# Kernel optimization log

Measured on AMD Instinct MI355X. Metric: run time of the kernel, lower is better.

Reference implementation:

```python
import jax, jax.numpy as jnp
import numpy as np

EPS = 1e-6


def ln_fwd(x, gamma, beta):
    # layernorm over last dim (biased variance), per TTT ln_fwd
    mu = x.mean(-1, keepdims=True)
    var = x.var(-1, keepdims=True)
    xh = (x - mu) * jax.lax.rsqrt(var + EPS)
    return gamma * xh + beta


def ln_fused_l2_bwd(x, l2_target, gamma, beta):
    # grad of 0.5*||LN(x) - target||^2 w.r.t. x, fused (per TTT ln_fused_l2_bwd)
    D = x.shape[-1]
    mu = x.mean(-1, keepdims=True)
    var = x.var(-1, keepdims=True)
    std = jnp.sqrt(var + EPS)
    xh = (x - mu) / std
    y = gamma * xh + beta
    gxh = (y - l2_target) * gamma
    z = (D * gxh - gxh.sum(-1, keepdims=True) - xh * (gxh * xh).sum(-1, keepdims=True)) / (D * std)
    return z


def setup_inputs() -> dict:
    key = jax.random.key(0)
    ks = jax.random.split(key, 5)
    B, nh, nmb, mbs, hd = 8, 8, 256, 16, 64
    XQ = jax.random.normal(ks[0], (B, nh, nmb, mbs, hd), jnp.float32)
    XK = jax.random.normal(ks[1], (B, nh, nmb, mbs, hd), jnp.float32)
    XV = jax.random.normal(ks[2], (B, nh, nmb, mbs, hd), jnp.float32)
    # eta = small positive per-token learning rates (ttt_base_lr/head_dim scale)
    eta = jax.random.uniform(ks[3], (B, nh, nmb, mbs, mbs), jnp.float32) * (1.0 / hd)
    W1 = jax.random.normal(ks[4], (nh, hd, hd), jnp.float32) * 0.02
    b1 = jnp.zeros((nh, 1, hd), jnp.float32)
    ln_weight = jnp.ones((nh * hd,), jnp.float32)
    ln_bias = jnp.zeros((nh * hd,), jnp.float32)
    return {"XQ": XQ, "XK": XK, "XV": XV, "eta": eta, "W1": W1, "b1": b1,
            "ln_weight": ln_weight, "ln_bias": ln_bias}


def reference(XQ, XK, XV, eta, W1, b1, ln_weight, ln_bias):
    B, nh, nmb, mbs, hd = XQ.shape
    lnw = ln_weight.reshape(nh, 1, hd)
    lnb = ln_bias.reshape(nh, 1, hd)
    W1_0 = jnp.broadcast_to(W1[None], (B, nh, hd, hd))
    b1_0 = jnp.broadcast_to(b1[None], (B, nh, 1, hd))
    tril = jnp.tril(jnp.ones((mbs, mbs), XQ.dtype))

    def step(carry, inp):
        W1s, b1s = carry               # [B,nh,hd,hd], [B,nh,1,hd]
        xq, xk, xv, et = inp           # [B,nh,mbs,hd] x3, [B,nh,mbs,mbs]
        Z1 = xk @ W1s + b1s
        g = ln_fused_l2_bwd(Z1, xv - xk, lnw, lnb)          # grad_l_wrt_Z1
        Attn1 = tril * (xq @ jnp.swapaxes(xk, -1, -2))      # causal QK^T
        b1_bar = b1s - (tril * et) @ g
        Z1_bar = xq @ W1s - (et * Attn1) @ g + b1_bar
        last_eta = et[..., -1, :, None]                     # [B,nh,mbs,1]
        W1_last = W1s - jnp.swapaxes(last_eta * xk, -1, -2) @ g
        b1_last = b1s - jnp.sum(last_eta * g, axis=-2, keepdims=True)
        out = xq + ln_fwd(Z1_bar, lnw, lnb)
        return (W1_last, b1_last), out

    xs = (jnp.moveaxis(XQ, 2, 0), jnp.moveaxis(XK, 2, 0),
          jnp.moveaxis(XV, 2, 0), jnp.moveaxis(eta, 2, 0))
    _, outs = jax.lax.scan(step, (W1_0, b1_0), xs)
    # outs: [nmb,B,nh,mbs,hd] -> [B,nmb,mbs,nh,hd] -> [B,L,width]
    return jnp.transpose(outs, (1, 0, 3, 2, 4)).reshape(B, nmb * mbs, nh * hd)
```

## Files before the change

### kernel.cpp

```cpp
#include <hip/hip_runtime.h>
#include <hip/hip_bf16.h>

typedef __attribute__((ext_vector_type(8))) short short8;
typedef __attribute__((ext_vector_type(4))) short short4_t;
typedef __attribute__((ext_vector_type(4))) float f32x4;

constexpr int MBS = 16, HD = 64, NMB = 256;

#define MFMA32(a, b, c) __builtin_amdgcn_mfma_f32_16x16x32_bf16(a, b, c, 0, 0, 0)

#if __has_builtin(__builtin_amdgcn_mfma_f32_16x16x16bf16_1k)
#define MFMA16(a, b, c) __builtin_amdgcn_mfma_f32_16x16x16bf16_1k(a, b, c, 0, 0, 0)
#else
__device__ inline f32x4 mfma16_asm(short4_t a, short4_t b, f32x4 c) {
    asm volatile("v_mfma_f32_16x16x16_bf16 %0, %1, %2, %0\n\ts_nop 7\n\ts_nop 7"
                 : "+v"(c) : "v"(a), "v"(b));
    return c;
}
#define MFMA16(a, b, c) mfma16_asm(a, b, c)
#endif

#define TR_READ(dst, addr, IMM) \
    asm volatile("ds_read_b64_tr_b16 %0, %1 offset:" IMM : "=&v"(dst) : "v"(addr) : "memory")

union U2S4 { unsigned u[2]; short4_t s; };
union FI { float f; int i; };

__device__ inline unsigned pkbf(float a, float b) {
    union { __hip_bfloat162 h; unsigned u; } c;
    c.h = __float22bfloat162_rn(make_float2(a, b));
    return c.u;
}
__device__ inline short bf16s(float x) { return (short)(pkbf(x, 0.f) & 0xffffu); }
__device__ inline float dpp16(float x) {
    FI v; v.f = x; FI t;
    t.i = __builtin_amdgcn_update_dpp(0, v.i, 0xB1, 0xf, 0xf, true);  v.f += t.f;
    t.i = __builtin_amdgcn_update_dpp(0, v.i, 0x4E, 0xf, 0xf, true);  v.f += t.f;
    t.i = __builtin_amdgcn_update_dpp(0, v.i, 0x124, 0xf, 0xf, true); v.f += t.f;
    t.i = __builtin_amdgcn_update_dpp(0, v.i, 0x128, 0xf, 0xf, true); v.f += t.f;
    return v.f;
}
__device__ inline void bar() {
    __builtin_amdgcn_sched_barrier(0);
    asm volatile("s_waitcnt lgkmcnt(0)" ::: "memory");
    __builtin_amdgcn_s_barrier();
    __builtin_amdgcn_sched_barrier(0);
}

__global__ __launch_bounds__(256) void ttt_scan(
    const float* __restrict__ gXQ, const float* __restrict__ gXK,
    const float* __restrict__ gXV, const float* __restrict__ gETA,
    const float* __restrict__ gW1, const float* __restrict__ gB1,
    const float* __restrict__ gLNW, const float* __restrict__ gLNB,
    float* __restrict__ gOUT)
{
    __shared__ __align__(16) short sWt[64 * 72];
    __shared__ __align__(16) short bxk[16 * 72];
    __shared__ __align__(16) short bxq[16 * 72];
    __shared__ __align__(16) short sGt[1024];
    __shared__ __align__(16) short sXKe[1024];
    __shared__ __align__(16) short sE[16 * 20];
    __shared__ __align__(16) float sZ1[16 * 68];
    __shared__ __align__(16) float sZb[16 * 68];
    __shared__ __align__(16) float sEta[2][256];

    const int t  = threadIdx.x;
    const int s  = t >> 4;
    const int dt = t & 15;
    const int lane = t & 63;
    const int w  = t >> 6;
    const int gq = lane >> 4;
    const int lc = lane & 15;
    const int bh = blockIdx.x, b = bh >> 3, h = bh & 7;

    const float* xqg = gXQ + (size_t)bh * (NMB * MBS * HD);
    const float* xkg = gXK + (size_t)bh * (NMB * MBS * HD);
    const float* xvg = gXV + (size_t)bh * (NMB * MBS * HD);
    const float* etg = gETA + (size_t)bh * (NMB * MBS * MBS);

    f32x4 Wacc[4];
#pragma unroll
    for (int ct = 0; ct < 4; ++ct) {
#pragma unroll
        for (int r = 0; r < 4; ++r)
            Wacc[ct][r] = gW1[h * 4096 + (16 * w + 4 * gq + r) * 64 + 16 * ct + lc];
        U2S4 wp;
        wp.u[0] = pkbf(Wacc[ct][0], Wacc[ct][1]);
        wp.u[1] = pkbf(Wacc[ct][2], Wacc[ct][3]);
        *(short4_t*)&sWt[(16 * ct + lc) * 72 + 16 * w + 4 * gq] = wp.s;
    }
    float b1v = gB1[h * 64 + 16 * w + lc];

    const float4 gam = *(const float4*)&gLNW[h * 64 + dt * 4];
    const float4 bet = *(const float4*)&gLNB[h * 64 + dt * 4];
    const float ga[4] = {gam.x, gam.y, gam.z, gam.w};
    const float ba[4] = {bet.x, bet.y, bet.z, bet.w};
    float c1a[4], gba[4];
    float sc1 = 0.f;
#pragma unroll
    for (int c = 0; c < 4; ++c) {
        c1a[c] = ga[c] * ga[c];
        gba[c] = ga[c] * ba[c];
        sc1 += c1a[c];
    }
    sc1 = dpp16(sc1);

    float4 pq = *(const float4*)&xqg[t * 4];
    float4 pk = *(const float4*)&xkg[t * 4];
    float4 pv = *(const float4*)&xvg[t * 4];
    float4 pe = make_float4(0.f, 0.f, 0.f, 0.f);
    if (t < 64) pe = *(const float4*)&etg[t * 4];

    { U2S4 u_; u_.u[0]=pkbf(pk.x,pk.y); u_.u[1]=pkbf(pk.z,pk.w);
      *(short4_t*)&bxk[s * 72 + dt * 4] = u_.s; }
    { U2S4 u_; u_.u[0]=pkbf(pq.x,pq.y); u_.u[1]=pkbf(pq.z,pq.w);
      *(short4_t*)&bxq[s * 72 + dt * 4] = u_.s; }
    if (t < 64) *(float4*)&sEta[0][t * 4] = pe;
    float t2c[4];
    {
        const float pva[4] = {pv.x, pv.y, pv.z, pv.w};
        const float pka_[4] = {pk.x, pk.y, pk.z, pk.w};
#pragma unroll
        for (int c = 0; c < 4; ++c)
            t2c[c] = fmaf(-ga[c], pva[c] - pka_[c], gba[c]);
    }
    float4 pkc = pk;
    float4 pq_out = pq;
    float4 pq_prev_out;

    __syncthreads();

#pragma unroll 1
    for (int m = 0; m < NMB; ++m) {
        const int p = m & 1;

        if (m + 1 < NMB) {
            const size_t o = (size_t)(m + 1) * (MBS * HD) + t * 4;
            pq = *(const float4*)&xqg[o];
            pk = *(const float4*)&xkg[o];
            pv = *(const float4*)&xvg[o];
            if (t < 64) pe = *(const float4*)&etg[(size_t)(m + 1) * (MBS * MBS) + t * 4];
        }

        f32x4 z1a; z1a[0]=b1v; z1a[1]=b1v; z1a[2]=b1v; z1a[3]=b1v;
        f32x4 zqa = z1a;
        const short8 ak0 = *(const short8*)&bxk[lc * 72 + gq * 8];
        const short8 ak1 = *(const short8*)&bxk[lc * 72 + gq * 8 + 32];
        const short8 aq0 = *(const short8*)&bxq[lc * 72 + gq * 8];
        const short8 aq1 = *(const short8*)&bxq[lc * 72 + gq * 8 + 32];
        const short8 bw0 = *(const short8*)&sWt[(16 * w + lc) * 72 + gq * 8];
        const short8 bw1 = *(const short8*)&sWt[(16 * w + lc) * 72 + gq * 8 + 32];
        z1a = MFMA32(ak0, bw0, z1a); z1a = MFMA32(ak1, bw1, z1a);
        zqa = MFMA32(aq0, bw0, zqa); zqa = MFMA32(aq1, bw1, zqa);
#pragma unroll
        for (int r = 0; r < 4; ++r) sZ1[(4 * gq + r) * 68 + 16 * w + lc] = z1a[r];

        if (w == 3) {
            f32x4 zz; zz[0]=0.f; zz[1]=0.f; zz[2]=0.f; zz[3]=0.f;
            zz = MFMA32(aq0, ak0, zz); zz = MFMA32(aq1, ak1, zz);
#pragma unroll
            for (int r = 0; r < 4; ++r) {
                const int row = 4 * gq + r;
                const float ev = sEta[p][row * 16 + lc];
                const float x = (lc <= row) ? -ev * (1.f + zz[r]) : 0.f;
                sE[row * 20 + lc] = bf16s(x);
            }
        }

        if (m > 0) {
            f32x4 zbr = *(f32x4*)&sZb[s * 68 + dt * 4];
            float T1 = 0.f, T2 = 0.f;
#pragma unroll
            for (int c = 0; c < 4; ++c) { T1 += zbr[c]; T2 = fmaf(zbr[c], zbr[c], T2); }
            T1 = dpp16(T1); T2 = dpp16(T2);
            const float mu2   = T1 * (1.f / 64.f);
            const float rstd2 = rsqrtf(T2 * (1.f / 64.f) - mu2 * mu2 + 1e-6f);
            const float pqa[4] = {pq_prev_out.x, pq_prev_out.y, pq_prev_out.z, pq_prev_out.w};
            float o[4];
#pragma unroll
            for (int c = 0; c < 4; ++c)
                o[c] = pqa[c] + fmaf(ga[c], (zbr[c] - mu2) * rstd2, ba[c]);
            const size_t oi = ((size_t)b * 4096 + (size_t)(m - 1) * 16 + s) * 512 + h * 64 + dt * 4;
            *(float4*)&gOUT[oi] = make_float4(o[0], o[1], o[2], o[3]);
        }
        bar();

        f32x4 z = *(f32x4*)&sZ1[s * 68 + dt * 4];
        float S1=0.f,S2=0.f,S3=0.f,S4=0.f,S5=0.f,S6=0.f;
#pragma unroll
        for (int c = 0; c < 4; ++c) {
            const float zc = z[c], c1z = c1a[c] * zc, t2 = t2c[c];
            S1 += zc;  S2 = fmaf(zc, zc, S2);
            S3 += c1z; S4 = fmaf(c1z, zc, S4);
            S5 += t2;  S6 = fmaf(t2, zc, S6);
        }
        S1 = dpp16(S1); S2 = dpp16(S2); S3 = dpp16(S3);
        S4 = dpp16(S4); S5 = dpp16(S5); S6 = dpp16(S6);
        const float mu   = S1 * (1.f / 64.f);
        const float rstd = rsqrtf(S2 * (1.f / 64.f) - mu * mu + 1e-6f);
        const float r1 = rstd * (S3 - mu * sc1) + S5;
        const float r2 = rstd * rstd * (S4 - 2.f * mu * S3 + mu * mu * sc1)
                       + rstd * (S6 - mu * S5);
        const float cf = rstd * (1.f / 64.f);
        float g[4];
#pragma unroll
        for (int c = 0; c < 4; ++c) {
            const float xh = (z[c] - mu) * rstd;
            const float gx = fmaf(c1a[c], xh, t2c[c]);
            g[c] = (fmaf(64.f, gx, -r1) - xh * r2) * cf;
        }

        const float le = sEta[p][240 + s];
        const int tb = (s >> 2) * 256 + (dt >> 2) * 64 + (s & 3) * 16 + (dt & 3) * 4;
        { U2S4 gp; gp.u[0]=pkbf(g[0],g[1]); gp.u[1]=pkbf(g[2],g[3]);
          *(short4_t*)&sGt[tb] = gp.s; }
        { U2S4 kp; kp.u[0]=pkbf(-le*pkc.x,-le*pkc.y); kp.u[1]=pkbf(-le*pkc.z,-le*pkc.w);
          *(short4_t*)&sXKe[tb] = kp.s; }
        bar();

        const unsigned gbase = (unsigned)(size_t)&sGt[0] + 512u * gq + 8u * lc;
        const unsigned kbase = (unsigned)(size_t)&sXKe[0] + 512u * gq + 128u * (unsigned)w + 8u * lc;
        short4_t bg0, bg1, bg2, bg3, aK;
        TR_READ(bg0, gbase, "0");
        TR_READ(bg1, gbase, "128");
        TR_READ(bg2, gbase, "256");
        TR_READ(bg3, gbase, "384");
        TR_READ(aK,  kbase, "0");
        const short4_t aE = *(const short4_t*)&sE[lc * 20 + gq * 4];
        const f32x4 lv = *(const f32x4*)&sEta[p][240 + 4 * gq];
        U2S4 aL;
        aL.u[0] = pkbf(-lv[0], -lv[1]);
        aL.u[1] = pkbf(-lv[2], -lv[3]);
        asm volatile("s_waitcnt lgkmcnt(0)" ::: "memory");
        __builtin_amdgcn_sched_barrier(0);

        short4_t bgw = bg0;
        if (w == 1) bgw = bg1;
        else if (w == 2) bgw = bg2;
        else if (w == 3) bgw = bg3;

        f32x4 zb = MFMA16(aE, bgw, zqa);
#pragma unroll
        for (int r = 0; r < 4; ++r) sZb[(4 * gq + r) * 68 + 16 * w + lc] = zb[r];

        Wacc[0] = MFMA16(aK, bg0, Wacc[0]);
        Wacc[1] = MFMA16(aK, bg1, Wacc[1]);
        Wacc[2] = MFMA16(aK, bg2, Wacc[2]);
        Wacc[3] = MFMA16(aK, bg3, Wacc[3]);
        {
            f32x4 d0; d0[0]=0.f; d0[1]=0.f; d0[2]=0.f; d0[3]=0.f;
            d0 = MFMA16(aL.s, bgw, d0);
            b1v += d0[0];
        }
#pragma unroll
        for (int ct = 0; ct < 4; ++ct) {
            U2S4 wp;
            wp.u[0] = pkbf(Wacc[ct][0], Wacc[ct][1]);
            wp.u[1] = pkbf(Wacc[ct][2], Wacc[ct][3]);
            *(short4_t*)&sWt[(16 * ct + lc) * 72 + 16 * w + 4 * gq] = wp.s;
        }

        if (m + 1 < NMB) {
            { U2S4 u_; u_.u[0]=pkbf(pk.x,pk.y); u_.u[1]=pkbf(pk.z,pk.w);
              *(short4_t*)&bxk[s * 72 + dt * 4] = u_.s; }
            { U2S4 u_; u_.u[0]=pkbf(pq.x,pq.y); u_.u[1]=pkbf(pq.z,pq.w);
              *(short4_t*)&bxq[s * 72 + dt * 4] = u_.s; }
            if (t < 64) *(float4*)&sEta[p ^ 1][t * 4] = pe;
#pragma unroll
            for (int c = 0; c < 4; ++c) {
                const float pva[4] = {pv.x, pv.y, pv.z, pv.w};
                const float pka_[4] = {pk.x, pk.y, pk.z, pk.w};
                t2c[c] = fmaf(-ga[c], pva[c] - pka_[c], gba[c]);
            }
            pkc = pk;
        }
        pq_prev_out = pq_out;
        pq_out = pq;
        bar();
    }

    {
        f32x4 zbr = *(f32x4*)&sZb[s * 68 + dt * 4];
        float T1 = 0.f, T2 = 0.f;
#pragma unroll
        for (int c = 0; c < 4; ++c) { T1 += zbr[c]; T2 = fmaf(zbr[c], zbr[c], T2); }
        T1 = dpp16(T1); T2 = dpp16(T2);
        const float mu2   = T1 * (1.f / 64.f);
        const float rstd2 = rsqrtf(T2 * (1.f / 64.f) - mu2 * mu2 + 1e-6f);
        const float pqa[4] = {pq_prev_out.x, pq_prev_out.y, pq_prev_out.z, pq_prev_out.w};
        float o[4];
#pragma unroll
        for (int c = 0; c < 4; ++c)
            o[c] = pqa[c] + fmaf(ga[c], (zbr[c] - mu2) * rstd2, ba[c]);
        const size_t oi = ((size_t)b * 4096 + (size_t)(NMB - 1) * 16 + s) * 512 + h * 64 + dt * 4;
        *(float4*)&gOUT[oi] = make_float4(o[0], o[1], o[2], o[3]);
    }
}

extern "C" void kernel_launch(void* const* d_in, const int* in_sizes, int n_in,
                              void* d_out, int out_size, void* d_ws, size_t ws_size,
                              hipStream_t stream) {
    const float* XQ  = (const float*)d_in[0];
    const float* XK  = (const float*)d_in[1];
    const float* XV  = (const float*)d_in[2];
    const float* ETA = (const float*)d_in[3];
    const float* W1  = (const float*)d_in[4];
    const float* B1  = (const float*)d_in[5];
    const float* LNW = (const float*)d_in[6];
    const float* LNB = (const float*)d_in[7];
    float* OUT = (float*)d_out;

    const int n_chains = in_sizes[0] / (NMB * MBS * HD);
    ttt_scan<<<n_chains, 256, 0, stream>>>(XQ, XK, XV, ETA, W1, B1, LNW, LNB, OUT);
}
```

Before: 374.7 us.

## Split scan block into producer and query warp groups with 512 threads

Doubles the block to 512 threads. The first 256 threads handle the key path: the Z1 matmul, the fused LN-L2 gradient and the W1 update. The other 256 handle the query path: the XQ@W and QK^T matmuls, the eta mask, the Z1_bar MFMA and the output layernorm and store. This spreads per-chunk work that one group of warps used to do serially across more waves, so the two paths can run concurrently between barriers. In exchange it costs extra barrier participants, duplicated b1 tracking, and more register pressure under the new launch bound.

```diff
diff --git a/kernel.cpp b/kernel.cpp
--- a/kernel.cpp
+++ b/kernel.cpp
@@ -47,7 +47,7 @@
     __builtin_amdgcn_sched_barrier(0);
 }
 
-__global__ __launch_bounds__(256) void ttt_scan(
+__global__ __launch_bounds__(512) void ttt_scan(
     const float* __restrict__ gXQ, const float* __restrict__ gXK,
     const float* __restrict__ gXV, const float* __restrict__ gETA,
     const float* __restrict__ gW1, const float* __restrict__ gB1,
@@ -65,10 +65,12 @@
     __shared__ __align__(16) float sEta[2][256];
 
     const int t  = threadIdx.x;
-    const int s  = t >> 4;
-    const int dt = t & 15;
-    const int lane = t & 63;
-    const int w  = t >> 6;
+    const bool prod = (t < 256);
+    const int t4 = t & 255;
+    const int s  = t4 >> 4;
+    const int dt = t4 & 15;
+    const int lane = t4 & 63;
+    const int w  = t4 >> 6;
     const int gq = lane >> 4;
     const int lc = lane & 15;
     const int bh = blockIdx.x, b = bh >> 3, h = bh & 7;
@@ -79,15 +81,17 @@
     const float* etg = gETA + (size_t)bh * (NMB * MBS * MBS);
 
     f32x4 Wacc[4];
-#pragma unroll
-    for (int ct = 0; ct < 4; ++ct) {
-#pragma unroll
-        for (int r = 0; r < 4; ++r)
-            Wacc[ct][r] = gW1[h * 4096 + (16 * w + 4 * gq + r) * 64 + 16 * ct + lc];
-        U2S4 wp;
-        wp.u[0] = pkbf(Wacc[ct][0], Wacc[ct][1]);
-        wp.u[1] = pkbf(Wacc[ct][2], Wacc[ct][3]);
-        *(short4_t*)&sWt[(16 * ct + lc) * 72 + 16 * w + 4 * gq] = wp.s;
+    if (prod) {
+#pragma unroll
+        for (int ct = 0; ct < 4; ++ct) {
+#pragma unroll
+            for (int r = 0; r < 4; ++r)
+                Wacc[ct][r] = gW1[h * 4096 + (16 * w + 4 * gq + r) * 64 + 16 * ct + lc];
+            U2S4 wp;
+            wp.u[0] = pkbf(Wacc[ct][0], Wacc[ct][1]);
+            wp.u[1] = pkbf(Wacc[ct][2], Wacc[ct][3]);
+            *(short4_t*)&sWt[(16 * ct + lc) * 72 + 16 * w + 4 * gq] = wp.s;
+        }
     }
     float b1v = gB1[h * 64 + 16 * w + lc];
 
@@ -105,181 +109,197 @@
     }
     sc1 = dpp16(sc1);
 
-    float4 pq = *(const float4*)&xqg[t * 4];
-    float4 pk = *(const float4*)&xkg[t * 4];
-    float4 pv = *(const float4*)&xvg[t * 4];
-    float4 pe = make_float4(0.f, 0.f, 0.f, 0.f);
-    if (t < 64) pe = *(const float4*)&etg[t * 4];
-
-    { U2S4 u_; u_.u[0]=pkbf(pk.x,pk.y); u_.u[1]=pkbf(pk.z,pk.w);
-      *(short4_t*)&bxk[s * 72 + dt * 4] = u_.s; }
-    { U2S4 u_; u_.u[0]=pkbf(pq.x,pq.y); u_.u[1]=pkbf(pq.z,pq.w);
-      *(short4_t*)&bxq[s * 72 + dt * 4] = u_.s; }
-    if (t < 64) *(float4*)&sEta[0][t * 4] = pe;
-    float t2c[4];
-    {
-        const float pva[4] = {pv.x, pv.y, pv.z, pv.w};
-        const float pka_[4] = {pk.x, pk.y, pk.z, pk.w};
-#pragma unroll
-        for (int c = 0; c < 4; ++c)
-            t2c[c] = fmaf(-ga[c], pva[c] - pka_[c], gba[c]);
-    }
-    float4 pkc = pk;
-    float4 pq_out = pq;
-    float4 pq_prev_out;
-
+    float4 pk_c, pv_c, pk_n, pv_n;
+    float4 pq_c, pq_n, pq_prev, pkb_n, pe_n;
+    if (prod) {
+        pk_c = *(const float4*)&xkg[t4 * 4];
+        pv_c = *(const float4*)&xvg[t4 * 4];
+    } else {
+        pq_c = *(const float4*)&xqg[t4 * 4];
+        float4 k0 = *(const float4*)&xkg[t4 * 4];
+        { U2S4 u_; u_.u[0]=pkbf(k0.x,k0.y); u_.u[1]=pkbf(k0.z,k0.w);
+          *(short4_t*)&bxk[s * 72 + dt * 4] = u_.s; }
+        { U2S4 u_; u_.u[0]=pkbf(pq_c.x,pq_c.y); u_.u[1]=pkbf(pq_c.z,pq_c.w);
+          *(short4_t*)&bxq[s * 72 + dt * 4] = u_.s; }
+        if (t4 < 64) {
+            float4 e0 = *(const float4*)&etg[t4 * 4];
+            *(float4*)&sEta[0][t4 * 4] = e0;
+        }
+    }
     __syncthreads();
 
 #pragma unroll 1
     for (int m = 0; m < NMB; ++m) {
         const int p = m & 1;
+        f32x4 zqa, zz;
 
         if (m + 1 < NMB) {
-            const size_t o = (size_t)(m + 1) * (MBS * HD) + t * 4;
-            pq = *(const float4*)&xqg[o];
-            pk = *(const float4*)&xkg[o];
-            pv = *(const float4*)&xvg[o];
-            if (t < 64) pe = *(const float4*)&etg[(size_t)(m + 1) * (MBS * MBS) + t * 4];
-        }
-
-        f32x4 z1a; z1a[0]=b1v; z1a[1]=b1v; z1a[2]=b1v; z1a[3]=b1v;
-        f32x4 zqa = z1a;
-        const short8 ak0 = *(const short8*)&bxk[lc * 72 + gq * 8];
-        const short8 ak1 = *(const short8*)&bxk[lc * 72 + gq * 8 + 32];
-        const short8 aq0 = *(const short8*)&bxq[lc * 72 + gq * 8];
-        const short8 aq1 = *(const short8*)&bxq[lc * 72 + gq * 8 + 32];
-        const short8 bw0 = *(const short8*)&sWt[(16 * w + lc) * 72 + gq * 8];
-        const short8 bw1 = *(const short8*)&sWt[(16 * w + lc) * 72 + gq * 8 + 32];
-        z1a = MFMA32(ak0, bw0, z1a); z1a = MFMA32(ak1, bw1, z1a);
-        zqa = MFMA32(aq0, bw0, zqa); zqa = MFMA32(aq1, bw1, zqa);
-#pragma unroll
-        for (int r = 0; r < 4; ++r) sZ1[(4 * gq + r) * 68 + 16 * w + lc] = z1a[r];
-
-        if (w == 3) {
-            f32x4 zz; zz[0]=0.f; zz[1]=0.f; zz[2]=0.f; zz[3]=0.f;
-            zz = MFMA32(aq0, ak0, zz); zz = MFMA32(aq1, ak1, zz);
-#pragma unroll
-            for (int r = 0; r < 4; ++r) {
-                const int row = 4 * gq + r;
-                const float ev = sEta[p][row * 16 + lc];
-                const float x = (lc <= row) ? -ev * (1.f + zz[r]) : 0.f;
-                sE[row * 20 + lc] = bf16s(x);
-            }
-        }
-
-        if (m > 0) {
-            f32x4 zbr = *(f32x4*)&sZb[s * 68 + dt * 4];
-            float T1 = 0.f, T2 = 0.f;
-#pragma unroll
-            for (int c = 0; c < 4; ++c) { T1 += zbr[c]; T2 = fmaf(zbr[c], zbr[c], T2); }
-            T1 = dpp16(T1); T2 = dpp16(T2);
-            const float mu2   = T1 * (1.f / 64.f);
-            const float rstd2 = rsqrtf(T2 * (1.f / 64.f) - mu2 * mu2 + 1e-6f);
-            const float pqa[4] = {pq_prev_out.x, pq_prev_out.y, pq_prev_out.z, pq_prev_out.w};
-            float o[4];
-#pragma unroll
-            for (int c = 0; c < 4; ++c)
-                o[c] = pqa[c] + fmaf(ga[c], (zbr[c] - mu2) * rstd2, ba[c]);
-            const size_t oi = ((size_t)b * 4096 + (size_t)(m - 1) * 16 + s) * 512 + h * 64 + dt * 4;
-            *(float4*)&gOUT[oi] = make_float4(o[0], o[1], o[2], o[3]);
+            const size_t o = (size_t)(m + 1) * (MBS * HD) + t4 * 4;
+            if (prod) {
+                pk_n = *(const float4*)&xkg[o];
+                pv_n = *(const float4*)&xvg[o];
+            } else {
+                pq_n  = *(const float4*)&xqg[o];
+                pkb_n = *(const float4*)&xkg[o];
+                if (t4 < 64)
+                    pe_n = *(const float4*)&etg[(size_t)(m + 1) * (MBS * MBS) + t4 * 4];
+            }
+        }
+        if (prod) {
+            f32x4 z1a; z1a[0]=b1v; z1a[1]=b1v; z1a[2]=b1v; z1a[3]=b1v;
+            const short8 ak0 = *(const short8*)&bxk[lc * 72 + gq * 8];
+            const short8 ak1 = *(const short8*)&bxk[lc * 72 + gq * 8 + 32];
+            const short8 bw0 = *(const short8*)&sWt[(16 * w + lc) * 72 + gq * 8];
+            const short8 bw1 = *(const short8*)&sWt[(16 * w + lc) * 72 + gq * 8 + 32];
+            z1a = MFMA32(ak0, bw0, z1a); z1a = MFMA32(ak1, bw1, z1a);
+#pragma unroll
+            for (int r = 0; r < 4; ++r) sZ1[(4 * gq + r) * 68 + 16 * w + lc] = z1a[r];
+        } else {
+            zqa[0]=b1v; zqa[1]=b1v; zqa[2]=b1v; zqa[3]=b1v;
+            const short8 aq0 = *(const short8*)&bxq[lc * 72 + gq * 8];
+            const short8 aq1 = *(const short8*)&bxq[lc * 72 + gq * 8 + 32];
+            const short8 bw0 = *(const short8*)&sWt[(16 * w + lc) * 72 + gq * 8];
+            const short8 bw1 = *(const short8*)&sWt[(16 * w + lc) * 72 + gq * 8 + 32];
+            zqa = MFMA32(aq0, bw0, zqa); zqa = MFMA32(aq1, bw1, zqa);
+            if (w == 3) {
+                const short8 ak0 = *(const short8*)&bxk[lc * 72 + gq * 8];
+                const short8 ak1 = *(const short8*)&bxk[lc * 72 + gq * 8 + 32];
+                zz[0]=0.f; zz[1]=0.f; zz[2]=0.f; zz[3]=0.f;
+                zz = MFMA32(aq0, ak0, zz); zz = MFMA32(aq1, ak1, zz);
+            }
+            if (m > 0) {
+                f32x4 zbr = *(f32x4*)&sZb[s * 68 + dt * 4];
+                float T1 = 0.f, T2 = 0.f;
+#pragma unroll
+                for (int c = 0; c < 4; ++c) { T1 += zbr[c]; T2 = fmaf(zbr[c], zbr[c], T2); }
+                T1 = dpp16(T1); T2 = dpp16(T2);
+                const float mu2   = T1 * (1.f / 64.f);
+                const float rstd2 = rsqrtf(T2 * (1.f / 64.f) - mu2 * mu2 + 1e-6f);
+                const float pqa[4] = {pq_prev.x, pq_prev.y, pq_prev.z, pq_prev.w};
+                float o[4];
+#pragma unroll
+                for (int c = 0; c < 4; ++c)
+                    o[c] = pqa[c] + fmaf(ga[c], (zbr[c] - mu2) * rstd2, ba[c]);
+                const size_t oi = ((size_t)b * 4096 + (size_t)(m - 1) * 16 + s) * 512 + h * 64 + dt * 4;
+                *(float4*)&gOUT[oi] = make_float4(o[0], o[1], o[2], o[3]);
+            }
         }
         bar();
 
-        f32x4 z = *(f32x4*)&sZ1[s * 68 + dt * 4];
-        float S1=0.f,S2=0.f,S3=0.f,S4=0.f,S5=0.f,S6=0.f;
-#pragma unroll
-        for (int c = 0; c < 4; ++c) {
-            const float zc = z[c], c1z = c1a[c] * zc, t2 = t2c[c];
-            S1 += zc;  S2 = fmaf(zc, zc, S2);
-            S3 += c1z; S4 = fmaf(c1z, zc, S4);
-            S5 += t2;  S6 = fmaf(t2, zc, S6);
-        }
-        S1 = dpp16(S1); S2 = dpp16(S2); S3 = dpp16(S3);
-        S4 = dpp16(S4); S5 = dpp16(S5); S6 = dpp16(S6);
-        const float mu   = S1 * (1.f / 64.f);
-        const float rstd = rsqrtf(S2 * (1.f / 64.f) - mu * mu + 1e-6f);
-        const float r1 = rstd * (S3 - mu * sc1) + S5;
-        const float r2 = rstd * rstd * (S4 - 2.f * mu * S3 + mu * mu * sc1)
-                       + rstd * (S6 - mu * S5);
-        const float cf = rstd * (1.f / 64.f);
-        float g[4];
-#pragma unroll
-        for (int c = 0; c < 4; ++c) {
-            const float xh = (z[c] - mu) * rstd;
-            const float gx = fmaf(c1a[c], xh, t2c[c]);
-            g[c] = (fmaf(64.f, gx, -r1) - xh * r2) * cf;
-        }
-
-        const float le = sEta[p][240 + s];
-        const int tb = (s >> 2) * 256 + (dt >> 2) * 64 + (s & 3) * 16 + (dt & 3) * 4;
-        { U2S4 gp; gp.u[0]=pkbf(g[0],g[1]); gp.u[1]=pkbf(g[2],g[3]);
-          *(short4_t*)&sGt[tb] = gp.s; }
-        { U2S4 kp; kp.u[0]=pkbf(-le*pkc.x,-le*pkc.y); kp.u[1]=pkbf(-le*pkc.z,-le*pkc.w);
-          *(short4_t*)&sXKe[tb] = kp.s; }
+        if (prod) {
+            float t2c[4];
+            {
+                const float pva[4] = {pv_c.x, pv_c.y, pv_c.z, pv_c.w};
+                const float pka_[4] = {pk_c.x, pk_c.y, pk_c.z, pk_c.w};
+#pragma unroll
+                for (int c = 0; c < 4; ++c)
+                    t2c[c] = fmaf(-ga[c], pva[c] - pka_[c], gba[c]);
+            }
+            f32x4 z = *(f32x4*)&sZ1[s * 68 + dt * 4];
+            float S1=0.f,S2=0.f,S3=0.f,S4=0.f,S5=0.f,S6=0.f;
+#pragma unroll
+            for (int c = 0; c < 4; ++c) {
+                const float zc = z[c], c1z = c1a[c] * zc, t2 = t2c[c];
+                S1 += zc;  S2 = fmaf(zc, zc, S2);
+                S3 += c1z; S4 = fmaf(c1z, zc, S4);
+                S5 += t2;  S6 = fmaf(t2, zc, S6);
+            }
+            S1 = dpp16(S1); S2 = dpp16(S2); S3 = dpp16(S3);
+            S4 = dpp16(S4); S5 = dpp16(S5); S6 = dpp16(S6);
+            const float mu   = S1 * (1.f / 64.f);
+            const float rstd = rsqrtf(S2 * (1.f / 64.f) - mu * mu + 1e-6f);
+            const float r1 = rstd * (S3 - mu * sc1) + S5;
+            const float r2 = rstd * rstd * (S4 - 2.f * mu * S3 + mu * mu * sc1)
+                           + rstd * (S6 - mu * S5);
+            const float cf = rstd * (1.f / 64.f);
+            float g[4];
+#pragma unroll
+            for (int c = 0; c < 4; ++c) {
+                const float xh = (z[c] - mu) * rstd;
+                const float gx = fmaf(c1a[c], xh, t2c[c]);
+                g[c] = (fmaf(64.f, gx, -r1) - xh * r2) * cf;
+            }
+            const float le = sEta[p][240 + s];
+            const int tb = (s >> 2) * 256 + (dt >> 2) * 64 + (s & 3) * 16 + (dt & 3) * 4;
+            { U2S4 gp; gp.u[0]=pkbf(g[0],g[1]); gp.u[1]=pkbf(g[2],g[3]);
+              *(short4_t*)&sGt[tb] = gp.s; }
+            { U2S4 kp; kp.u[0]=pkbf(-le*pk_c.x,-le*pk_c.y); kp.u[1]=pkbf(-le*pk_c.z,-le*pk_c.w);
+              *(short4_t*)&sXKe[tb] = kp.s; }
+            pk_c = pk_n; pv_c = pv_n;
+        } else {
+            if (m + 1 < NMB) {
+                { U2S4 u_; u_.u[0]=pkbf(pkb_n.x,pkb_n.y); u_.u[1]=pkbf(pkb_n.z,pkb_n.w);
+                  *(short4_t*)&bxk[s * 72 + dt * 4] = u_.s; }
+                { U2S4 u_; u_.u[0]=pkbf(pq_n.x,pq_n.y); u_.u[1]=pkbf(pq_n.z,pq_n.w);
+                  *(short4_t*)&bxq[s * 72 + dt * 4] = u_.s; }
+                if (t4 < 64) *(float4*)&sEta[p ^ 1][t4 * 4] = pe_n;
+            }
+            if (w == 3) {
+#pragma unroll
+                for (int r = 0; r < 4; ++r) {
+                    const int row = 4 * gq + r;
+                    const float ev = sEta[p][row * 16 + lc];
+                    const float x = (lc <= row) ? -ev * (1.f + zz[r]) : 0.f;
+                    sE[row * 20 + lc] = bf16s(x);
+                }
+            }
+            pq_prev = pq_c; pq_c = pq_n;
+        }
         bar();
 
         const unsigned gbase = (unsigned)(size_t)&sGt[0] + 512u * gq + 8u * lc;
-        const unsigned kbase = (unsigned)(size_t)&sXKe[0] + 512u * gq + 128u * (unsigned)w + 8u * lc;
-        short4_t bg0, bg1, bg2, bg3, aK;
-        TR_READ(bg0, gbase, "0");
-        TR_READ(bg1, gbase, "128");
-        TR_READ(bg2, gbase, "256");
-        TR_READ(bg3, gbase, "384");
-        TR_READ(aK,  kbase, "0");
-        const short4_t aE = *(const short4_t*)&sE[lc * 20 + gq * 4];
         const f32x4 lv = *(const f32x4*)&sEta[p][240 + 4 * gq];
         U2S4 aL;
         aL.u[0] = pkbf(-lv[0], -lv[1]);
         aL.u[1] = pkbf(-lv[2], -lv[3]);
-        asm volatile("s_waitcnt lgkmcnt(0)" ::: "memory");
-        __builtin_amdgcn_sched_barrier(0);
-
-        short4_t bgw = bg0;
-        if (w == 1) bgw = bg1;
-        else if (w == 2) bgw = bg2;
-        else if (w == 3) bgw = bg3;
-
-        f32x4 zb = MFMA16(aE, bgw, zqa);
-#pragma unroll
-        for (int r = 0; r < 4; ++r) sZb[(4 * gq + r) * 68 + 16 * w + lc] = zb[r];
-
-        Wacc[0] = MFMA16(aK, bg0, Wacc[0]);
-        Wacc[1] = MFMA16(aK, bg1, Wacc[1]);
-        Wacc[2] = MFMA16(aK, bg2, Wacc[2]);
-        Wacc[3] = MFMA16(aK, bg3, Wacc[3]);
-        {
+        if (prod) {
+            const unsigned kbase = (unsigned)(size_t)&sXKe[0] + 512u * gq + 128u * (unsigned)w + 8u * lc;
+            short4_t bg0, bg1, bg2, bg3, aK;
+            TR_READ(bg0, gbase, "0");
+            TR_READ(bg1, gbase, "128");
+            TR_READ(bg2, gbase, "256");
+            TR_READ(bg3, gbase, "384");
+            TR_READ(aK,  kbase, "0");
+            asm volatile("s_waitcnt lgkmcnt(0)" ::: "memory");
+            __builtin_amdgcn_sched_barrier(0);
+
+            Wacc[0] = MFMA16(aK, bg0, Wacc[0]);
+            Wacc[1] = MFMA16(aK, bg1, Wacc[1]);
+            Wacc[2] = MFMA16(aK, bg2, Wacc[2]);
+            Wacc[3] = MFMA16(aK, bg3, Wacc[3]);
+            short4_t bgw = bg0;
+            if (w == 1) bgw = bg1;
+            else if (w == 2) bgw = bg2;
+            else if (w == 3) bgw = bg3;
             f32x4 d0; d0[0]=0.f; d0[1]=0.f; d0[2]=0.f; d0[3]=0.f;
             d0 = MFMA16(aL.s, bgw, d0);
             b1v += d0[0];
-        }
-#pragma unroll
-        for (int ct = 0; ct < 4; ++ct) {
-            U2S4 wp;
-            wp.u[0] = pkbf(Wacc[ct][0], Wacc[ct][1]);
-            wp.u[1] = pkbf(Wacc[ct][2], Wacc[ct][3]);
-            *(short4_t*)&sWt[(16 * ct + lc) * 72 + 16 * w + 4 * gq] = wp.s;
-        }
-
-        if (m + 1 < NMB) {
-            { U2S4 u_; u_.u[0]=pkbf(pk.x,pk.y); u_.u[1]=pkbf(pk.z,pk.w);
-              *(short4_t*)&bxk[s * 72 + dt * 4] = u_.s; }
-            { U2S4 u_; u_.u[0]=pkbf(pq.x,pq.y); u_.u[1]=pkbf(pq.z,pq.w);
-              *(short4_t*)&bxq[s * 72 + dt * 4] = u_.s; }
-            if (t < 64) *(float4*)&sEta[p ^ 1][t * 4] = pe;
-#pragma unroll
-            for (int c = 0; c < 4; ++c) {
-                const float pva[4] = {pv.x, pv.y, pv.z, pv.w};
-                const float pka_[4] = {pk.x, pk.y, pk.z, pk.w};
-                t2c[c] = fmaf(-ga[c], pva[c] - pka_[c], gba[c]);
-            }
-            pkc = pk;
-        }
-        pq_prev_out = pq_out;
-        pq_out = pq;
+#pragma unroll
+            for (int ct = 0; ct < 4; ++ct) {
+                U2S4 wp;
+                wp.u[0] = pkbf(Wacc[ct][0], Wacc[ct][1]);
+                wp.u[1] = pkbf(Wacc[ct][2], Wacc[ct][3]);
+                *(short4_t*)&sWt[(16 * ct + lc) * 72 + 16 * w + 4 * gq] = wp.s;
+            }
+        } else {
+            short4_t bgw;
+            const unsigned gbw = gbase + 128u * (unsigned)w;
+            TR_READ(bgw, gbw, "0");
+            const short4_t aE = *(const short4_t*)&sE[lc * 20 + gq * 4];
+            asm volatile("s_waitcnt lgkmcnt(0)" ::: "memory");
+            __builtin_amdgcn_sched_barrier(0);
+
+            f32x4 zb = MFMA16(aE, bgw, zqa);
+#pragma unroll
+            for (int r = 0; r < 4; ++r) sZb[(4 * gq + r) * 68 + 16 * w + lc] = zb[r];
+            f32x4 d0; d0[0]=0.f; d0[1]=0.f; d0[2]=0.f; d0[3]=0.f;
+            d0 = MFMA16(aL.s, bgw, d0);
+            b1v += d0[0];
+        }
         bar();
     }
 
-    {
+    if (!prod) {
         f32x4 zbr = *(f32x4*)&sZb[s * 68 + dt * 4];
         float T1 = 0.f, T2 = 0.f;
 #pragma unroll
@@ -287,7 +307,7 @@
         T1 = dpp16(T1); T2 = dpp16(T2);
         const float mu2   = T1 * (1.f / 64.f);
         const float rstd2 = rsqrtf(T2 * (1.f / 64.f) - mu2 * mu2 + 1e-6f);
-        const float pqa[4] = {pq_prev_out.x, pq_prev_out.y, pq_prev_out.z, pq_prev_out.w};
+        const float pqa[4] = {pq_prev.x, pq_prev.y, pq_prev.z, pq_prev.w};
         float o[4];
 #pragma unroll
         for (int c = 0; c < 4; ++c)
@@ -311,5 +331,5 @@
     float* OUT = (float*)d_out;
 
     const int n_chains = in_sizes[0] / (NMB * MBS * HD);
-    ttt_scan<<<n_chains, 256, 0, stream>>>(XQ, XK, XV, ETA, W1, B1, LNW, LNB, OUT);
-}
+    ttt_scan<<<n_chains, 512, 0, stream>>>(XQ, XK, XV, ETA, W1, B1, LNW, LNB, OUT);
+}
```

Result: no change. 374.4 us (-0.1%).
